# Kernel optimization log

Measured on AMD Instinct MI355X. Metric: run time of the kernel, lower is better.

## Reference

```python
import math
import jax, jax.numpy as jnp
import numpy as np

D_MODEL = 1024
NHEAD = 16
HEAD_DIM = D_MODEL // NHEAD
BATCH = 2
SEQ = 2048


def setup_inputs() -> dict:
    key = jax.random.key(0)
    ks = jax.random.split(key, 8)
    data = jax.random.normal(ks[0], (BATCH, SEQ, D_MODEL), dtype=jnp.float32)
    temporal = jax.random.uniform(ks[1], (BATCH, SEQ), dtype=jnp.float32)
    mask = jnp.zeros((SEQ, SEQ), dtype=jnp.float32)
    s = 1.0 / math.sqrt(D_MODEL)
    Wq = jax.random.normal(ks[2], (D_MODEL, D_MODEL), dtype=jnp.float32) * s
    Wk = jax.random.normal(ks[3], (D_MODEL, D_MODEL), dtype=jnp.float32) * s
    Wv = jax.random.normal(ks[4], (D_MODEL, D_MODEL), dtype=jnp.float32) * s
    bq = jax.random.normal(ks[5], (D_MODEL,), dtype=jnp.float32) * 0.02
    bk = jax.random.normal(ks[6], (D_MODEL,), dtype=jnp.float32) * 0.02
    bv = jax.random.normal(ks[7], (D_MODEL,), dtype=jnp.float32) * 0.02
    return {"data": data, "temporal": temporal, "mask": mask,
            "Wq": Wq, "bq": bq, "Wk": Wk, "bk": bk, "Wv": Wv, "bv": bv}


def _rotate_half_pairs(x):
    # x: [..., s] with s even; pairs (x0,x1) -> (-x1, x0) interleaved
    x2 = x.reshape(x.shape[:-1] + (-1, 2))  # [..., s//2, 2]
    rot = jnp.stack([-x2[..., 1], x2[..., 0]], axis=-1)
    return rot.reshape(x.shape)


def reference(data, temporal, mask, Wq, bq, Wk, bk, Wv, bv):
    B, L, D = data.shape
    H, S = NHEAD, HEAD_DIM
    scale = math.sqrt(S)

    query = (data @ Wq + bq).reshape(B, L, H, S)
    key_ = (data @ Wk + bk).reshape(B, L, H, S)
    value = (data @ Wv + bv).reshape(B, L, H, S)

    # freq = 10000^(-arange(0, S, 2)/S), repeat_interleave(2) -> [S]
    freq = jnp.power(10000.0, -jnp.arange(0, S, 2, dtype=jnp.float32) / S)
    freq = jnp.repeat(freq, 2)
    freqs = temporal[:, :, None] * freq[None, None, :]  # [B, L, S]
    cosine = jnp.cos(freqs)[:, :, None, :]  # [B, L, 1, S]
    sine = jnp.sin(freqs)[:, :, None, :]

    rq = query * cosine + _rotate_half_pairs(query) * sine
    rk = key_ * cosine + _rotate_half_pairs(key_) * sine

    logits = jnp.einsum('bqhs,bkhs->bhqk', rq, rk) / scale
    logits = logits + mask  # mask: [L, L], broadcasts over b,h
    weights = jax.nn.softmax(logits, axis=-1)
    context = jnp.einsum('bhqk,bkhs->bqhs', weights, value)
    return context.reshape(B, L, D)
```

## Files before the change

### kernel.cpp

```cpp
#include <hip/hip_runtime.h>
#include <hip/hip_bf16.h>

#define D_MODEL 1024
#define NHEAD   16
#define HEAD_DIM 64
#define BATCH   2
#define SEQ     2048
#define NTOK    (BATCH*SEQ)

#define FREQ_LOG2 0.20762050593046015f

typedef short  bfrag __attribute__((ext_vector_type(8)));
typedef float  ffrag __attribute__((ext_vector_type(4)));

__device__ inline ushort f2bf(float x) {
    __hip_bfloat16 h = __float2bfloat16(x);
    return __builtin_bit_cast(ushort, h);
}
__device__ inline float bf2f(ushort u) {
    return __builtin_bit_cast(float, (uint)u << 16);
}
__device__ inline void split_bf(float x, ushort& hi, ushort& lo) {
    __hip_bfloat16 h = __float2bfloat16(x);
    hi = __builtin_bit_cast(ushort, h);
    lo = f2bf(x - __bfloat162float(h));
}

__device__ inline void gload16(const ushort* g, ushort* l) {
    __builtin_amdgcn_global_load_lds(
        (const __attribute__((address_space(1))) void*)g,
        (__attribute__((address_space(3))) void*)l, 16, 0, 0);
}

__global__ __launch_bounds__(256)
void split_data(const float* __restrict__ x, ushort* __restrict__ hi,
                ushort* __restrict__ lo)
{
    const int i4 = (blockIdx.x * 256 + threadIdx.x) * 4;
    const float4 v = *(const float4*)(x + i4);
    ushort4 h, l;
    split_bf(v.x, h.x, l.x); split_bf(v.y, h.y, l.y);
    split_bf(v.z, h.z, l.z); split_bf(v.w, h.w, l.w);
    *(ushort4*)(hi + i4) = h;
    *(ushort4*)(lo + i4) = l;
}

__global__ __launch_bounds__(256)
void mask_bf(const float* __restrict__ m, ushort* __restrict__ o)
{
    const int i4 = (blockIdx.x * 256 + threadIdx.x) * 4;
    const float4 v = *(const float4*)(m + i4);
    ushort4 h;
    h.x = f2bf(v.x); h.y = f2bf(v.y); h.z = f2bf(v.z); h.w = f2bf(v.w);
    *(ushort4*)(o + i4) = h;
}

__global__ __launch_bounds__(256)
void split_tr_w(const float* __restrict__ Wq, const float* __restrict__ Wk,
                const float* __restrict__ Wv, ushort* __restrict__ hi)
{
    const int z = blockIdx.z;
    const float* W = (z == 0) ? Wq : (z == 1) ? Wk : Wv;
    ushort* thi = hi + (size_t)z * D_MODEL * D_MODEL;

    __shared__ float T[64][65];
    const int t  = threadIdx.x;
    const int k0 = blockIdx.x * 64, n0 = blockIdx.y * 64;

    #pragma unroll
    for (int i = 0; i < 4; i++) {
        const int f = i * 256 + t, r = f >> 4, c = (f & 15) * 4;
        const float4 v = *(const float4*)(W + (size_t)(k0 + r) * D_MODEL + n0 + c);
        T[r][c] = v.x; T[r][c + 1] = v.y; T[r][c + 2] = v.z; T[r][c + 3] = v.w;
    }
    __syncthreads();
    #pragma unroll
    for (int i = 0; i < 4; i++) {
        const int f = i * 256 + t, nr = f >> 4, kc = (f & 15) * 4;
        ushort4 h;
        h.x = f2bf(T[kc + 0][nr]);
        h.y = f2bf(T[kc + 1][nr]);
        h.z = f2bf(T[kc + 2][nr]);
        h.w = f2bf(T[kc + 3][nr]);
        const size_t o = (size_t)(n0 + nr) * D_MODEL + k0 + kc;
        *(ushort4*)(thi + o) = h;
    }
}

#define BK 32

union GemmSM {
    ushort st[2][3][128 * BK];
    float  c[64 * 132];
};

__global__ __launch_bounds__(256, 3)
void gemm_qkv(const ushort* __restrict__ Ahi, const ushort* __restrict__ Alo,
              const ushort* __restrict__ WThi,
              const float* __restrict__ bq, const float* __restrict__ bk,
              const float* __restrict__ bv, const float* __restrict__ temporal,
              ushort* __restrict__ Qhi, ushort* __restrict__ Qlo,
              ushort* __restrict__ Khi,
              ushort* __restrict__ VT)
{
    __shared__ GemmSM sm;
    const int z  = blockIdx.z;
    const int m0 = blockIdx.x * 128;
    const int n0 = blockIdx.y * 128;
    const float* bias = (z == 0) ? bq : (z == 1) ? bk : bv;
    const ushort* Bh = WThi + (size_t)z * D_MODEL * D_MODEL;

    const int t = threadIdx.x;
    const int w = t >> 6, lane = t & 63;
    const int lane15 = lane & 15, quad8 = (lane >> 4) * 8, quad = lane >> 4;
    const int wm = (w >> 1) * 64, wn = (w & 1) * 64;

    ffrag acc[4][4];
    #pragma unroll
    for (int i = 0; i < 4; i++)
        #pragma unroll
        for (int j = 0; j < 4; j++) acc[i][j] = (ffrag){0.f, 0.f, 0.f, 0.f};

    const int wr = w * 32;
    const int lr = lane >> 2;
    const int lc = (((lane & 3) ^ ((lane >> 3) & 3))) * 8;

    auto stage = [&](int bsel, int k0) {
        #pragma unroll
        for (int ch = 0; ch < 2; ch++) {
            const int rb = wr + ch * 16;
            const ushort* ga = Ahi + (size_t)(m0 + rb + lr) * D_MODEL + k0 + lc;
            const ushort* gl = Alo + (size_t)(m0 + rb + lr) * D_MODEL + k0 + lc;
            const ushort* gb = Bh  + (size_t)(n0 + rb + lr) * D_MODEL + k0 + lc;
            gload16(ga, &sm.st[bsel][0][rb * BK]);
            gload16(gl, &sm.st[bsel][1][rb * BK]);
            gload16(gb, &sm.st[bsel][2][rb * BK]);
        }
    };

    stage(0, 0);
    __syncthreads();

    const int rdsw = (quad ^ ((lane15 >> 1) & 3)) * 8;

    int buf = 0;
    for (int k0 = 0; k0 < D_MODEL; k0 += BK) {
        if (k0 + BK < D_MODEL) stage(buf ^ 1, k0 + BK);

        bfrag ah[4], al[4];
        #pragma unroll
        for (int mt = 0; mt < 4; mt++) {
            ah[mt] = *(const bfrag*)&sm.st[buf][0][(wm + mt * 16 + lane15) * BK + rdsw];
            al[mt] = *(const bfrag*)&sm.st[buf][1][(wm + mt * 16 + lane15) * BK + rdsw];
        }
        #pragma unroll
        for (int nt = 0; nt < 4; nt++) {
            const bfrag bh = *(const bfrag*)&sm.st[buf][2][(wn + nt * 16 + lane15) * BK + rdsw];
            #pragma unroll
            for (int mt = 0; mt < 4; mt++) {
                ffrag a = acc[mt][nt];
                a = __builtin_amdgcn_mfma_f32_16x16x32_bf16(ah[mt], bh, a, 0, 0, 0);
                a = __builtin_amdgcn_mfma_f32_16x16x32_bf16(al[mt], bh, a, 0, 0, 0);
                acc[mt][nt] = a;
            }
        }
        __syncthreads();
        buf ^= 1;
    }

    float bn[4];
    #pragma unroll
    for (int nt = 0; nt < 4; nt++) bn[nt] = bias[n0 + wn + nt * 16 + lane15];

    const int CST = (z == 2) ? 129 : 132;

    #pragma unroll
    for (int p = 0; p < 2; p++) {
        if (p) __syncthreads();
        if ((w >> 1) == p) {
            #pragma unroll
            for (int mt = 0; mt < 4; mt++)
                #pragma unroll
                for (int nt = 0; nt < 4; nt++)
                    #pragma unroll
                    for (int rr = 0; rr < 4; rr++)
                        sm.c[(mt * 16 + quad * 4 + rr) * CST + wn + nt * 16 + lane15] =
                            acc[mt][nt][rr] + bn[nt];
        }
        __syncthreads();

        if (z < 2) {
            ushort* ohi = (z == 0) ? Qhi : Khi;
            const float sc = (z == 0) ? 0.125f : 1.0f;
            #pragma unroll
            for (int i = 0; i < 8; i++) {
                const int f = i * 256 + t, r = f >> 5, c4 = (f & 31) * 4;
                float4 v = *(float4*)&sm.c[r * 132 + c4];
                const int m = m0 + p * 64 + r;
                const float tv = temporal[m];
                const float fr0 = exp2f(-(float)(c4 & 63) * FREQ_LOG2);
                const float fr1 = exp2f(-(float)((c4 + 2) & 63) * FREQ_LOG2);
                float s0, c0, s1, c1v;
                __sincosf(tv * fr0, &s0, &c0);
                __sincosf(tv * fr1, &s1, &c1v);
                const float y0 = (v.x * c0 - v.y * s0) * sc;
                const float y1 = (v.y * c0 + v.x * s0) * sc;
                const float y2 = (v.z * c1v - v.w * s1) * sc;
                const float y3 = (v.w * c1v + v.z * s1) * sc;
                ushort4 h, l;
                split_bf(y0, h.x, l.x); split_bf(y1, h.y, l.y);
                split_bf(y2, h.z, l.z); split_bf(y3, h.w, l.w);
                const size_t o = (size_t)m * D_MODEL + n0 + c4;
                *(ushort4*)(ohi + o) = h;
                if (z == 0) *(ushort4*)(Qlo + o) = l;
            }
        } else {
            const int bb = m0 >> 11;
            #pragma unroll
            for (int i = 0; i < 4; i++) {
                const int cid = i * 256 + t, col = cid >> 3, tg = (cid & 7) * 8;
                ushort u8[8];
                #pragma unroll
                for (int j = 0; j < 8; j++) u8[j] = f2bf(sm.c[(tg + j) * 129 + col]);
                const int ncol = n0 + col, hh = ncol >> 6, d = ncol & 63;
                const size_t dst = ((size_t)(bb * NHEAD + hh) * HEAD_DIM + d) * SEQ +
                                   (m0 & (SEQ - 1)) + p * 64 + tg;
                *(int4*)(VT + dst) = *(int4*)u8;
            }
        }
    }
}

__global__ __launch_bounds__(256, 2)
void attn_mfma(const ushort* __restrict__ Qhi, const ushort* __restrict__ Qlo,
               const ushort* __restrict__ Khi,
               const ushort* __restrict__ VT,  const ushort* __restrict__ maskbf,
               float* __restrict__ out)
{
    __shared__ ushort lsK[2][64 * 64], lsV[2][64 * 64], lsP[128 * 64];

    const int bid  = blockIdx.x;
    const int bh   = (bid & 7) * 4 + (bid >> 7);
    const int qb   = (bid >> 3) & 15;
    const int b    = bh >> 4, h = bh & 15;
    const int q0   = qb * 128;

    const int t = threadIdx.x, w = t >> 6, lane = t & 63;
    const int lane15 = lane & 15, quad = lane >> 4;
    const size_t tok0 = (size_t)b * SEQ;

    bfrag qh[2][2], ql[2][2];
    #pragma unroll
    for (int su = 0; su < 2; su++) {
        const size_t qrow = (tok0 + q0 + w * 32 + su * 16 + lane15) * D_MODEL +
                            h * HEAD_DIM;
        #pragma unroll
        for (int ks = 0; ks < 2; ks++) {
            qh[su][ks] = *(const bfrag*)(Qhi + qrow + ks * 32 + quad * 8);
            ql[su][ks] = *(const bfrag*)(Qlo + qrow + ks * 32 + quad * 8);
        }
    }

    ffrag of[2][4];
    float l_i[2][4];
    #pragma unroll
    for (int su = 0; su < 2; su++)
        #pragma unroll
        for (int nt = 0; nt < 4; nt++) {
            of[su][nt] = (ffrag){0.f, 0.f, 0.f, 0.f};
            l_i[su][nt] = 0.f;
        }

    const int r1 = t >> 3,  c1 = (t & 7) * 8;
    const int sw = ((t & 7) ^ (r1 & 7)) * 8;
    const ushort* Kh0 = Khi + tok0 * D_MODEL + h * HEAD_DIM;
    const ushort* Vt0 = VT + (size_t)(b * NHEAD + h) * HEAD_DIM * SEQ;

    int4 pk0 = *(const int4*)(Kh0 + (size_t)r1 * D_MODEL + c1);
    int4 pk1 = *(const int4*)(Kh0 + (size_t)(32 + r1) * D_MODEL + c1);
    int4 pv0 = *(const int4*)(Vt0 + (size_t)r1 * SEQ + c1);
    int4 pv1 = *(const int4*)(Vt0 + (size_t)(32 + r1) * SEQ + c1);

    *(int4*)&lsK[0][r1 * 64 + sw]        = pk0;
    *(int4*)&lsK[0][(32 + r1) * 64 + sw] = pk1;
    *(int4*)&lsV[0][r1 * 64 + sw]        = pv0;
    *(int4*)&lsV[0][(32 + r1) * 64 + sw] = pv1;

    pk0 = *(const int4*)(Kh0 + (size_t)(64 + r1) * D_MODEL + c1);
    pk1 = *(const int4*)(Kh0 + (size_t)(96 + r1) * D_MODEL + c1);
    pv0 = *(const int4*)(Vt0 + (size_t)r1 * SEQ + 64 + c1);
    pv1 = *(const int4*)(Vt0 + (size_t)(32 + r1) * SEQ + 64 + c1);
    __syncthreads();

    const ushort* mrow0 = maskbf + (size_t)(q0 + w * 32 + quad * 4) * SEQ;
    const ushort* mrow1 = maskbf + (size_t)(q0 + w * 32 + 16 + quad * 4) * SEQ;

    const int krd  = lane15 & 7;
    const int keyr = (((lane15 >> 2) & 3) << 1) | (lane15 & 1);

    int cur = 0;
    for (int kt = 0; kt < SEQ; kt += 64) {
        if (kt + 64 < SEQ) {
            *(int4*)&lsK[cur ^ 1][r1 * 64 + sw]        = pk0;
            *(int4*)&lsK[cur ^ 1][(32 + r1) * 64 + sw] = pk1;
            *(int4*)&lsV[cur ^ 1][r1 * 64 + sw]        = pv0;
            *(int4*)&lsV[cur ^ 1][(32 + r1) * 64 + sw] = pv1;
        }

        float mv0[4][4], mv1[4][4];
        #pragma unroll
        for (int nt = 0; nt < 4; nt++)
            #pragma unroll
            for (int rr = 0; rr < 4; rr++) {
                mv0[nt][rr] = bf2f(mrow0[(size_t)rr * SEQ + kt + nt * 16 + lane15]);
                mv1[nt][rr] = bf2f(mrow1[(size_t)rr * SEQ + kt + nt * 16 + lane15]);
            }

        const int ktn = (kt + 128 < SEQ) ? kt + 128 : 0;
        pk0 = *(const int4*)(Kh0 + (size_t)(ktn + r1) * D_MODEL + c1);
        pk1 = *(const int4*)(Kh0 + (size_t)(ktn + 32 + r1) * D_MODEL + c1);
        pv0 = *(const int4*)(Vt0 + (size_t)r1 * SEQ + ktn + c1);
        pv1 = *(const int4*)(Vt0 + (size_t)(32 + r1) * SEQ + ktn + c1);

        ffrag s0[4], s1[4];
        #pragma unroll
        for (int nt = 0; nt < 4; nt++) {
            const bfrag kf0 = *(const bfrag*)&lsK[cur][(nt * 16 + lane15) * 64 +
                                                       ((0 + quad) ^ krd) * 8];
            const bfrag kf1 = *(const bfrag*)&lsK[cur][(nt * 16 + lane15) * 64 +
                                                       ((4 + quad) ^ krd) * 8];
            ffrag a0 = (ffrag){0.f, 0.f, 0.f, 0.f};
            ffrag a1 = (ffrag){0.f, 0.f, 0.f, 0.f};
            a0 = __builtin_amdgcn_mfma_f32_16x16x32_bf16(qh[0][0], kf0, a0, 0, 0, 0);
            a0 = __builtin_amdgcn_mfma_f32_16x16x32_bf16(ql[0][0], kf0, a0, 0, 0, 0);
            a0 = __builtin_amdgcn_mfma_f32_16x16x32_bf16(qh[0][1], kf1, a0, 0, 0, 0);
            a0 = __builtin_amdgcn_mfma_f32_16x16x32_bf16(ql[0][1], kf1, a0, 0, 0, 0);
            a1 = __builtin_amdgcn_mfma_f32_16x16x32_bf16(qh[1][0], kf0, a1, 0, 0, 0);
            a1 = __builtin_amdgcn_mfma_f32_16x16x32_bf16(ql[1][0], kf0, a1, 0, 0, 0);
            a1 = __builtin_amdgcn_mfma_f32_16x16x32_bf16(qh[1][1], kf1, a1, 0, 0, 0);
            a1 = __builtin_amdgcn_mfma_f32_16x16x32_bf16(ql[1][1], kf1, a1, 0, 0, 0);
            s0[nt] = a0;
            s1[nt] = a1;
        }

        #pragma unroll
        for (int nt = 0; nt < 4; nt++)
            #pragma unroll
            for (int rr = 0; rr < 4; rr++) {
                const int pchk = (2 * nt + (lane15 >> 3)) ^ ((quad << 1) | (rr & 1));
                const float e0 = __expf(s0[nt][rr] + mv0[nt][rr]);
                l_i[0][rr] += e0;
                lsP[(w * 32 + quad * 4 + rr) * 64 + pchk * 8 + (lane15 & 7)] = f2bf(e0);
                const float e1 = __expf(s1[nt][rr] + mv1[nt][rr]);
                l_i[1][rr] += e1;
                lsP[(w * 32 + 16 + quad * 4 + rr) * 64 + pchk * 8 + (lane15 & 7)] = f2bf(e1);
            }

        #pragma unroll
        for (int ks = 0; ks < 2; ks++) {
            const bfrag pf0 = *(const bfrag*)&lsP[(w * 32 + lane15) * 64 +
                                                  ((ks * 4 + quad) ^ keyr) * 8];
            const bfrag pf1 = *(const bfrag*)&lsP[(w * 32 + 16 + lane15) * 64 +
                                                  ((ks * 4 + quad) ^ keyr) * 8];
            #pragma unroll
            for (int nt = 0; nt < 4; nt++) {
                const bfrag vf = *(const bfrag*)&lsV[cur][(nt * 16 + lane15) * 64 +
                                                          ((ks * 4 + quad) ^ krd) * 8];
                of[0][nt] = __builtin_amdgcn_mfma_f32_16x16x32_bf16(pf0, vf, of[0][nt], 0, 0, 0);
                of[1][nt] = __builtin_amdgcn_mfma_f32_16x16x32_bf16(pf1, vf, of[1][nt], 0, 0, 0);
            }
        }

        __syncthreads();
        cur ^= 1;
    }

    #pragma unroll
    for (int su = 0; su < 2; su++) {
        float inv[4];
        #pragma unroll
        for (int rr = 0; rr < 4; rr++) {
            float v = l_i[su][rr];
            #pragma unroll
            for (int off = 1; off < 16; off <<= 1) v += __shfl_xor(v, off);
            inv[rr] = 1.0f / v;
        }
        #pragma unroll
        for (int nt = 0; nt < 4; nt++)
            #pragma unroll
            for (int rr = 0; rr < 4; rr++)
                out[(tok0 + q0 + w * 32 + su * 16 + quad * 4 + rr) * D_MODEL +
                    h * HEAD_DIM + nt * 16 + lane15] = of[su][nt][rr] * inv[rr];
    }
}

extern "C" void kernel_launch(void* const* d_in, const int* in_sizes, int n_in,
                              void* d_out, int out_size, void* d_ws, size_t ws_size,
                              hipStream_t stream)
{
    const float* data     = (const float*)d_in[0];
    const float* temporal = (const float*)d_in[1];
    const float* mask     = (const float*)d_in[2];
    const float* Wq = (const float*)d_in[3];
    const float* bq = (const float*)d_in[4];
    const float* Wk = (const float*)d_in[5];
    const float* bk = (const float*)d_in[6];
    const float* Wv = (const float*)d_in[7];
    const float* bv = (const float*)d_in[8];
    float* out = (float*)d_out;

    char* ws = (char*)d_ws;
    const size_t MB = 1024 * 1024;
    ushort* Ahi  = (ushort*)(ws + 0 * MB);
    ushort* Alo  = (ushort*)(ws + 8 * MB);
    ushort* WThi = (ushort*)(ws + 16 * MB);
    ushort* Qhi  = (ushort*)(ws + 28 * MB);
    ushort* Qlo  = (ushort*)(ws + 36 * MB);
    ushort* Khi  = (ushort*)(ws + 44 * MB);
    ushort* VT   = (ushort*)(ws + 60 * MB);
    ushort* Mbf  = (ushort*)(ws + 68 * MB);

    split_data<<<dim3(NTOK * D_MODEL / 1024), 256, 0, stream>>>(data, Ahi, Alo);
    mask_bf<<<dim3(SEQ * SEQ / 1024), 256, 0, stream>>>(mask, Mbf);
    split_tr_w<<<dim3(16, 16, 3), 256, 0, stream>>>(Wq, Wk, Wv, WThi);
    gemm_qkv<<<dim3(NTOK / 128, D_MODEL / 128, 3), 256, 0, stream>>>(
        Ahi, Alo, WThi, bq, bk, bv, temporal,
        Qhi, Qlo, Khi, VT);
    attn_mfma<<<dim3(BATCH * NHEAD * SEQ / 128), 256, 0, stream>>>(
        Qhi, Qlo, Khi, VT, Mbf, out);
}
```

Before: 261.9 us.

## Merge prep kernels, remap GEMM blocks per XCD, raise MFMA wave priority

Folds the three preprocessing kernels (data split, mask conversion, weight transpose) into one launch that dispatches on block index, cutting launch overhead and gaps between launches. The QKV GEMM grid is flattened to 1D and remapped so blocks landing on the same XCD share M rows and weight tiles, aiming for better L2 reuse. In the attention kernel, s_setprio raises wave priority around the MFMA sections to favour matrix-core issue over other waves. The merged prep kernel allocates shared memory for every block, including the element-wise ones, which may lower their occupancy.

```diff
diff --git a/kernel.cpp b/kernel.cpp
--- a/kernel.cpp
+++ b/kernel.cpp
@@ -33,39 +33,39 @@
 }
 
 __global__ __launch_bounds__(256)
-void split_data(const float* __restrict__ x, ushort* __restrict__ hi,
-                ushort* __restrict__ lo)
+void prep(const float* __restrict__ data, ushort* __restrict__ Ahi,
+          ushort* __restrict__ Alo,
+          const float* __restrict__ mask, ushort* __restrict__ Mbf,
+          const float* __restrict__ Wq, const float* __restrict__ Wk,
+          const float* __restrict__ Wv, ushort* __restrict__ WThi)
 {
-    const int i4 = (blockIdx.x * 256 + threadIdx.x) * 4;
-    const float4 v = *(const float4*)(x + i4);
-    ushort4 h, l;
-    split_bf(v.x, h.x, l.x); split_bf(v.y, h.y, l.y);
-    split_bf(v.z, h.z, l.z); split_bf(v.w, h.w, l.w);
-    *(ushort4*)(hi + i4) = h;
-    *(ushort4*)(lo + i4) = l;
-}
-
-__global__ __launch_bounds__(256)
-void mask_bf(const float* __restrict__ m, ushort* __restrict__ o)
-{
-    const int i4 = (blockIdx.x * 256 + threadIdx.x) * 4;
-    const float4 v = *(const float4*)(m + i4);
-    ushort4 h;
-    h.x = f2bf(v.x); h.y = f2bf(v.y); h.z = f2bf(v.z); h.w = f2bf(v.w);
-    *(ushort4*)(o + i4) = h;
-}
-
-__global__ __launch_bounds__(256)
-void split_tr_w(const float* __restrict__ Wq, const float* __restrict__ Wk,
-                const float* __restrict__ Wv, ushort* __restrict__ hi)
-{
-    const int z = blockIdx.z;
+    __shared__ float T[64][65];
+    const int bid = blockIdx.x, t = threadIdx.x;
+
+    if (bid < 4096) {
+        const int i4 = (bid * 256 + t) * 4;
+        const float4 v = *(const float4*)(data + i4);
+        ushort4 h, l;
+        split_bf(v.x, h.x, l.x); split_bf(v.y, h.y, l.y);
+        split_bf(v.z, h.z, l.z); split_bf(v.w, h.w, l.w);
+        *(ushort4*)(Ahi + i4) = h;
+        *(ushort4*)(Alo + i4) = l;
+        return;
+    }
+    if (bid < 8192) {
+        const int i4 = ((bid - 4096) * 256 + t) * 4;
+        const float4 v = *(const float4*)(mask + i4);
+        ushort4 h;
+        h.x = f2bf(v.x); h.y = f2bf(v.y); h.z = f2bf(v.z); h.w = f2bf(v.w);
+        *(ushort4*)(Mbf + i4) = h;
+        return;
+    }
+    const int id  = bid - 8192;
+    const int z   = id >> 8;
+    const int rem = id & 255;
+    const int k0  = (rem & 15) * 64, n0 = (rem >> 4) * 64;
     const float* W = (z == 0) ? Wq : (z == 1) ? Wk : Wv;
-    ushort* thi = hi + (size_t)z * D_MODEL * D_MODEL;
-
-    __shared__ float T[64][65];
-    const int t  = threadIdx.x;
-    const int k0 = blockIdx.x * 64, n0 = blockIdx.y * 64;
+    ushort* thi = WThi + (size_t)z * D_MODEL * D_MODEL;
 
     #pragma unroll
     for (int i = 0; i < 4; i++) {
@@ -104,9 +104,13 @@
               ushort* __restrict__ VT)
 {
     __shared__ GemmSM sm;
-    const int z  = blockIdx.z;
-    const int m0 = blockIdx.x * 128;
-    const int n0 = blockIdx.y * 128;
+    const int bidl = blockIdx.x;
+    const int xcd  = bidl & 7, kk = bidl >> 3;
+    const int m0   = (xcd * 4 + (kk & 3)) * 128;
+    const int nz   = kk >> 2;
+    const int n0   = (nz & 7) * 128;
+    const int z    = nz >> 3;
+
     const float* bias = (z == 0) ? bq : (z == 1) ? bk : bv;
     const ushort* Bh = WThi + (size_t)z * D_MODEL * D_MODEL;
 
@@ -323,6 +327,7 @@
         pv1 = *(const int4*)(Vt0 + (size_t)(32 + r1) * SEQ + ktn + c1);
 
         ffrag s0[4], s1[4];
+        __builtin_amdgcn_s_setprio(1);
         #pragma unroll
         for (int nt = 0; nt < 4; nt++) {
             const bfrag kf0 = *(const bfrag*)&lsK[cur][(nt * 16 + lane15) * 64 +
@@ -342,6 +347,7 @@
             s0[nt] = a0;
             s1[nt] = a1;
         }
+        __builtin_amdgcn_s_setprio(0);
 
         #pragma unroll
         for (int nt = 0; nt < 4; nt++)
@@ -356,6 +362,7 @@
                 lsP[(w * 32 + 16 + quad * 4 + rr) * 64 + pchk * 8 + (lane15 & 7)] = f2bf(e1);
             }
 
+        __builtin_amdgcn_s_setprio(1);
         #pragma unroll
         for (int ks = 0; ks < 2; ks++) {
             const bfrag pf0 = *(const bfrag*)&lsP[(w * 32 + lane15) * 64 +
@@ -370,6 +377,7 @@
                 of[1][nt] = __builtin_amdgcn_mfma_f32_16x16x32_bf16(pf1, vf, of[1][nt], 0, 0, 0);
             }
         }
+        __builtin_amdgcn_s_setprio(0);
 
         __syncthreads();
         cur ^= 1;
@@ -420,10 +428,9 @@
     ushort* VT   = (ushort*)(ws + 60 * MB);
     ushort* Mbf  = (ushort*)(ws + 68 * MB);
 
-    split_data<<<dim3(NTOK * D_MODEL / 1024), 256, 0, stream>>>(data, Ahi, Alo);
-    mask_bf<<<dim3(SEQ * SEQ / 1024), 256, 0, stream>>>(mask, Mbf);
-    split_tr_w<<<dim3(16, 16, 3), 256, 0, stream>>>(Wq, Wk, Wv, WThi);
-    gemm_qkv<<<dim3(NTOK / 128, D_MODEL / 128, 3), 256, 0, stream>>>(
+    prep<<<dim3(8960), 256, 0, stream>>>(data, Ahi, Alo, mask, Mbf,
+                                         Wq, Wk, Wv, WThi);
+    gemm_qkv<<<dim3(768), 256, 0, stream>>>(
         Ahi, Alo, WThi, bq, bk, bv, temporal,
         Qhi, Qlo, Khi, VT);
     attn_mfma<<<dim3(BATCH * NHEAD * SEQ / 128), 256, 0, stream>>>(
```

Measured after the change: 258.6 us. No clear change (-1.3%).
